# Kernel tuning notes

Hardware: AMD Instinct MI355X
Metric: run time of the kernel (lower is better)

Reference implementation:

```python
import jax, jax.numpy as jnp
import numpy as np
from math import sqrt

B, S, D, H = 2, 2048, 1024, 16
HD = D // H


def setup_inputs() -> dict:
    key = jax.random.key(0)
    ks = jax.random.split(key, 5)
    std = 0.02
    return {
        "tensor_in": jax.random.normal(ks[0], (B, S, D), dtype=jnp.float32),
        "attention_mask": jnp.zeros((1, 1, S, S), dtype=jnp.float32),
        "Wq": jax.random.normal(ks[1], (D, D), dtype=jnp.float32) * std,
        "Wk": jax.random.normal(ks[2], (D, D), dtype=jnp.float32) * std,
        "Wv": jax.random.normal(ks[3], (D, D), dtype=jnp.float32) * std,
        "Wo": jax.random.normal(ks[4], (D, D), dtype=jnp.float32) * std,
    }


def reference(tensor_in, attention_mask, Wq, Wk, Wv, Wo):
    # nn.Linear(dim, dim, bias=False): y = x @ W.T, W is [out, in]
    q = tensor_in @ Wq.T  # [B,S,D]
    k = tensor_in @ Wk.T
    v = tensor_in @ Wv.T
    # split heads -> [B,H,S,HD]
    q = q.reshape(B, S, H, HD).transpose(0, 2, 1, 3)
    k = k.reshape(B, S, H, HD).transpose(0, 2, 1, 3)
    v = v.reshape(B, S, H, HD).transpose(0, 2, 1, 3)
    # scores [B,H,S,S]; note: mask added BEFORE scaling, scale = sqrt(full dim)
    scores = jnp.einsum("bhqd,bhkd->bhqk", q, k) + attention_mask
    weights = jax.nn.softmax(scores / sqrt(D), axis=-1)  # dropout = identity (eval)
    context = jnp.einsum("bhqk,bhkd->bhqd", weights, v)
    context = context.transpose(0, 2, 1, 3).reshape(B, S, D)
    return context @ Wo.T
```

## Files before the change

kernel.cpp:

```cpp
#include <hip/hip_runtime.h>

#define B_  2
#define S_  2048
#define D_  1024
#define H_  16
#define HD_ 64
#define M_  (B_*S_)

typedef __attribute__((ext_vector_type(8))) short  short8;
typedef __attribute__((ext_vector_type(4))) float  float4v;
typedef __attribute__((ext_vector_type(4))) int    int4v;
typedef __attribute__((ext_vector_type(4))) unsigned short ushort4v;

#define PSCALE 0.0450843341f

__device__ __forceinline__ unsigned int pack2_bf16(float a, float b) {
#if __has_builtin(__builtin_amdgcn_cvt_pk_bf16_f32)
    auto p = __builtin_amdgcn_cvt_pk_bf16_f32(a, b);
    return __builtin_bit_cast(unsigned int, p);
#else
    unsigned int xa = __builtin_bit_cast(unsigned int, a);
    unsigned int xb = __builtin_bit_cast(unsigned int, b);
    xa += 0x7fffu + ((xa >> 16) & 1u);
    xb += 0x7fffu + ((xb >> 16) & 1u);
    return (xa >> 16) | (xb & 0xffff0000u);
#endif
}
__device__ __forceinline__ unsigned short f_to_bf16bits(float f) {
#if __has_builtin(__builtin_amdgcn_cvt_pk_bf16_f32)
    return (unsigned short)(pack2_bf16(f, f) & 0xffffu);
#else
    unsigned int x = __builtin_bit_cast(unsigned int, f);
    x += 0x7fffu + ((x >> 16) & 1u);
    return (unsigned short)(x >> 16);
#endif
}

__device__ __forceinline__ float fast_exp2(float x) {
#if __has_builtin(__builtin_amdgcn_exp2f)
    return __builtin_amdgcn_exp2f(x);
#else
    return exp2f(x);
#endif
}

__global__ __launch_bounds__(256) void cvt_bf16(
    const float* __restrict__ X,  const float* __restrict__ Wq,
    const float* __restrict__ Wk, const float* __restrict__ Wv,
    const float* __restrict__ Wo,
    unsigned short* __restrict__ Xb,  unsigned short* __restrict__ Wqb,
    unsigned short* __restrict__ Wkb, unsigned short* __restrict__ Wvb,
    unsigned short* __restrict__ Wob)
{
    const long t = (long)blockIdx.x * 256 + threadIdx.x;
    const long e = t * 8;
    const float* src; unsigned short* dst; long off;
    if      (e < 4194304) { src = X;  dst = Xb;  off = e; }
    else if (e < 5242880) { src = Wq; dst = Wqb; off = e - 4194304; }
    else if (e < 6291456) { src = Wk; dst = Wkb; off = e - 5242880; }
    else if (e < 7340032) { src = Wv; dst = Wvb; off = e - 6291456; }
    else                  { src = Wo; dst = Wob; off = e - 7340032; }
    float4v a = *(const float4v*)&src[off];
    float4v b = *(const float4v*)&src[off + 4];
    int4v o;
    o[0] = (int)pack2_bf16(a[0], a[1]);
    o[1] = (int)pack2_bf16(a[2], a[3]);
    o[2] = (int)pack2_bf16(b[0], b[1]);
    o[3] = (int)pack2_bf16(b[2], b[3]);
    *(int4v*)&dst[off] = o;
}

__global__ __launch_bounds__(256) void gemm_bt(
    const unsigned short* __restrict__ A,
    const unsigned short* __restrict__ B0,
    const unsigned short* __restrict__ B1,
    const unsigned short* __restrict__ B2,
    void* __restrict__ O0, void* __restrict__ O1, void* __restrict__ O2,
    int mode_base)
{
    const int K = 1024;
    const int z = blockIdx.z;
    const int mode = mode_base + z;
    const unsigned short* Aop;
    const unsigned short* Bop;
    void* Op = (z == 0) ? O0 : (z == 1) ? O1 : O2;
    int m0, n0;
    if (mode == 2) {
        Aop = B2; Bop = A;
        m0 = blockIdx.y * 128;
        n0 = blockIdx.x * 128;
    } else {
        Aop = A;
        Bop = (z == 0) ? B0 : (z == 1) ? B1 : B2;
        m0 = blockIdx.x * 128;
        n0 = blockIdx.y * 128;
    }

    __shared__ alignas(16) unsigned short As[128 * 64];
    __shared__ alignas(16) unsigned short Bs[128 * 64];

    const int tid  = threadIdx.x;
    const int wv   = tid >> 6;
    const int lane = tid & 63;
    const int wm   = wv >> 1, wn = wv & 1;
    const int q4   = lane >> 4, l15 = lane & 15;

    const unsigned short* gA[4];
    const unsigned short* gB[4];
    int ldsoff[4];
#pragma unroll
    for (int j = 0; j < 4; j++) {
        const int r = wv * 32 + j * 8 + (lane >> 3);
        const int c = (((lane & 7) ^ (r & 7)) * 8);
        gA[j] = Aop + (long)(m0 + r) * K + c;
        gB[j] = Bop + (long)(n0 + r) * K + c;
        ldsoff[j] = (wv * 32 + j * 8) * 64 + lane * 8;
    }

    int aoff[2][4], boff[2][4];
#pragma unroll
    for (int ks = 0; ks < 2; ks++)
#pragma unroll
        for (int t = 0; t < 4; t++) {
            const int swz = (((ks * 4 + q4) ^ (l15 & 7)) * 8);
            aoff[ks][t] = (wm * 64 + t * 16 + l15) * 64 + swz;
            boff[ks][t] = (wn * 64 + t * 16 + l15) * 64 + swz;
        }

    float4v acc[4][4];
#pragma unroll
    for (int i = 0; i < 4; i++)
#pragma unroll
        for (int j = 0; j < 4; j++) acc[i][j] = (float4v)0.0f;

    int4v ar[4], br[4];
#pragma unroll
    for (int j = 0; j < 4; j++) {
        ar[j] = *(const int4v*)gA[j];
        br[j] = *(const int4v*)gB[j];
        gA[j] += 64; gB[j] += 64;
    }

    for (int k0 = 0; k0 < K; k0 += 64) {
        __syncthreads();
#pragma unroll
        for (int j = 0; j < 4; j++) {
            *(int4v*)&As[ldsoff[j]] = ar[j];
            *(int4v*)&Bs[ldsoff[j]] = br[j];
        }
        __syncthreads();

        if (k0 + 64 < K) {
#pragma unroll
            for (int j = 0; j < 4; j++) {
                ar[j] = *(const int4v*)gA[j];
                br[j] = *(const int4v*)gB[j];
                gA[j] += 64; gB[j] += 64;
            }
        }

#pragma unroll
        for (int ks = 0; ks < 2; ks++) {
            short8 afr[4], bfr[4];
#pragma unroll
            for (int mt = 0; mt < 4; mt++) afr[mt] = *(const short8*)&As[aoff[ks][mt]];
#pragma unroll
            for (int nt = 0; nt < 4; nt++) bfr[nt] = *(const short8*)&Bs[boff[ks][nt]];
#pragma unroll
            for (int mt = 0; mt < 4; mt++)
#pragma unroll
                for (int nt = 0; nt < 4; nt++)
                    acc[mt][nt] = __builtin_amdgcn_mfma_f32_16x16x32_bf16(
                        afr[mt], bfr[nt], acc[mt][nt], 0, 0, 0);
        }
    }

#pragma unroll
    for (int mt = 0; mt < 4; mt++)
#pragma unroll
        for (int nt = 0; nt < 4; nt++)
#pragma unroll
            for (int r = 0; r < 4; r++) {
                const int m = m0 + wm * 64 + mt * 16 + q4 * 4 + r;
                const int n = n0 + wn * 64 + nt * 16 + l15;
                float v = acc[mt][nt][r];
                if (mode == 3) {
                    ((float*)Op)[(long)m * D_ + n] = v;
                } else if (mode == 2) {
                    const long off = (((long)(n >> 11) * H_ + (m >> 6)) * HD_ + (m & 63)) * S_ + (n & 2047);
                    ((unsigned short*)Op)[off] = f_to_bf16bits(v);
                } else {
                    const long off = ((long)((m >> 11) * H_ + (n >> 6)) * S_ + (m & 2047)) * HD_ + (n & 63);
                    if (mode == 0) v *= PSCALE;
                    ((unsigned short*)Op)[off] = f_to_bf16bits(v);
                }
            }
}

__global__ __launch_bounds__(128) void attn(
    const unsigned short* __restrict__ Q,
    const unsigned short* __restrict__ Kk,
    const unsigned short* __restrict__ Vt,
    const float* __restrict__ mask,
    unsigned short* __restrict__ ctx)
{
    __shared__ alignas(16) unsigned short Ks [64 * 72];
    __shared__ alignas(16) unsigned short Vts[64 * 72];
    __shared__ alignas(16) unsigned short Ps [2][32 * 72];

    const int tid  = threadIdx.x;
    const int wv   = tid >> 6;
    const int lane = tid & 63;
    const int q4   = lane >> 4, l15 = lane & 15;
    const int bh   = blockIdx.y;
    const int q0   = blockIdx.x * 64;

    const long head = (long)bh * S_ * HD_;

    short8 qfr[2][2];
#pragma unroll
    for (int mt = 0; mt < 2; mt++) {
        const int qrow = q0 + wv * 32 + mt * 16 + l15;
        qfr[mt][0] = *(const short8*)&Q[head + (long)qrow * HD_ + q4 * 8];
        qfr[mt][1] = *(const short8*)&Q[head + (long)qrow * HD_ + 32 + q4 * 8];
    }

    float l_acc[2][4];
#pragma unroll
    for (int mt = 0; mt < 2; mt++)
#pragma unroll
        for (int r = 0; r < 4; r++) l_acc[mt][r] = 0.0f;
    float4v oacc[2][4];
#pragma unroll
    for (int mt = 0; mt < 2; mt++)
#pragma unroll
        for (int dt = 0; dt < 4; dt++) oacc[mt][dt] = (float4v)0.0f;

    const int srow = tid >> 3;
    const int scol = (tid & 7) * 8;
    const unsigned short* gK[4];
    const unsigned short* gV[4];
    int ldsOff[4];
#pragma unroll
    for (int j = 0; j < 4; j++) {
        const int row = j * 16 + srow;
        gK[j] = Kk + head + (long)row * HD_ + scol;
        gV[j] = Vt + head + (long)row * S_  + scol;
        ldsOff[j] = row * 72 + scol;
    }

    const float* mrow[2][4];
#pragma unroll
    for (int mt = 0; mt < 2; mt++)
#pragma unroll
        for (int r = 0; r < 4; r++)
            mrow[mt][r] = mask + (long)(q0 + wv * 32 + mt * 16 + q4 * 4 + r) * S_ + l15;

    for (int k0 = 0; k0 < S_; k0 += 64) {
        __syncthreads();
#pragma unroll
        for (int j = 0; j < 4; j++) {
            *(int4v*)&Ks [ldsOff[j]] = *(const int4v*)(gK[j] + (long)k0 * HD_);
            *(int4v*)&Vts[ldsOff[j]] = *(const int4v*)(gV[j] + k0);
        }
        __syncthreads();

        float mv[2][4][4];
#pragma unroll
        for (int mt = 0; mt < 2; mt++)
#pragma unroll
            for (int nt = 0; nt < 4; nt++)
#pragma unroll
                for (int r = 0; r < 4; r++)
                    mv[mt][nt][r] = mrow[mt][r][k0 + nt * 16];

        float4v sfr[2][4];
#pragma unroll
        for (int nt = 0; nt < 4; nt++) {
            short8 kb0 = *(const short8*)&Ks[(nt * 16 + l15) * 72 + q4 * 8];
            short8 kb1 = *(const short8*)&Ks[(nt * 16 + l15) * 72 + 32 + q4 * 8];
#pragma unroll
            for (int mt = 0; mt < 2; mt++) {
                float4v s = (float4v)0.0f;
                s = __builtin_amdgcn_mfma_f32_16x16x32_bf16(qfr[mt][0], kb0, s, 0, 0, 0);
                s = __builtin_amdgcn_mfma_f32_16x16x32_bf16(qfr[mt][1], kb1, s, 0, 0, 0);
                sfr[mt][nt] = s;
            }
        }

#pragma unroll
        for (int mt = 0; mt < 2; mt++)
#pragma unroll
            for (int nt = 0; nt < 4; nt++)
#pragma unroll
                for (int r = 0; r < 4; r++) {
                    const float p = fast_exp2(fmaf(mv[mt][nt][r], PSCALE, sfr[mt][nt][r]));
                    l_acc[mt][r] += p;
                    Ps[wv][(mt * 16 + q4 * 4 + r) * 72 + nt * 16 + l15] = f_to_bf16bits(p);
                }

        short8 pf[2][2];
#pragma unroll
        for (int mt = 0; mt < 2; mt++) {
            pf[mt][0] = *(const short8*)&Ps[wv][(mt * 16 + l15) * 72 + q4 * 8];
            pf[mt][1] = *(const short8*)&Ps[wv][(mt * 16 + l15) * 72 + 32 + q4 * 8];
        }

#pragma unroll
        for (int dt = 0; dt < 4; dt++) {
            short8 vb0 = *(const short8*)&Vts[(dt * 16 + l15) * 72 + q4 * 8];
            short8 vb1 = *(const short8*)&Vts[(dt * 16 + l15) * 72 + 32 + q4 * 8];
#pragma unroll
            for (int mt = 0; mt < 2; mt++) {
                float4v o = oacc[mt][dt];
                o = __builtin_amdgcn_mfma_f32_16x16x32_bf16(pf[mt][0], vb0, o, 0, 0, 0);
                o = __builtin_amdgcn_mfma_f32_16x16x32_bf16(pf[mt][1], vb1, o, 0, 0, 0);
                oacc[mt][dt] = o;
            }
        }
    }

#pragma unroll
    for (int mt = 0; mt < 2; mt++)
#pragma unroll
        for (int r = 0; r < 4; r++) {
#pragma unroll
            for (int off = 1; off < 16; off <<= 1)
                l_acc[mt][r] += __shfl_xor(l_acc[mt][r], off);
        }

    const int b = bh >> 4, h = bh & 15;
#pragma unroll
    for (int mt = 0; mt < 2; mt++)
#pragma unroll
        for (int dt = 0; dt < 4; dt++)
#pragma unroll
            for (int r = 0; r < 4; r++) {
                const int qg = q0 + wv * 32 + mt * 16 + q4 * 4 + r;
                const int d  = dt * 16 + l15;
                const float v = oacc[mt][dt][r] / l_acc[mt][r];
                ctx[((long)(b * S_ + qg)) * D_ + h * HD_ + d] = f_to_bf16bits(v);
            }
}

extern "C" void kernel_launch(void* const* d_in, const int* in_sizes, int n_in,
                              void* d_out, int out_size, void* d_ws, size_t ws_size,
                              hipStream_t stream) {
    const float* X    = (const float*)d_in[0];
    const float* mask = (const float*)d_in[1];
    const float* Wq   = (const float*)d_in[2];
    const float* Wk   = (const float*)d_in[3];
    const float* Wv   = (const float*)d_in[4];
    const float* Wo   = (const float*)d_in[5];
    float* out        = (float*)d_out;

    unsigned short* ws = (unsigned short*)d_ws;
    unsigned short* qws  = ws;
    unsigned short* kws  = ws + 4194304;
    unsigned short* vtws = ws + 8388608;
    unsigned short* ctx  = ws + 12582912;
    unsigned short* Xb   = ws + 16777216;
    unsigned short* Wqb  = ws + 20971520;
    unsigned short* Wkb  = ws + 22020096;
    unsigned short* Wvb  = ws + 23068672;
    unsigned short* Wob  = ws + 24117248;

    cvt_bf16<<<dim3(4096), 256, 0, stream>>>(X, Wq, Wk, Wv, Wo, Xb, Wqb, Wkb, Wvb, Wob);
    gemm_bt<<<dim3(32, 8, 3), 256, 0, stream>>>(Xb, Wqb, Wkb, Wvb, qws, kws, vtws, 0);
    attn<<<dim3(32, 32, 1), 128, 0, stream>>>(qws, kws, vtws, mask, ctx);
    gemm_bt<<<dim3(32, 8, 1), 256, 0, stream>>>(ctx, Wob, Wob, Wob, out, out, out, 3);
}
```

Before: 225.6 us.

## Keep softmax probabilities in registers via permlane swaps and prefetch K/V tiles

The attention kernel now computes S transposed (K as the A operand). Each lane then holds four consecutive key columns, so probabilities are packed to bf16 in registers and rearranged with permlane32/16 swaps into the PV MFMA A-operand layout. This removes the per-wave LDS round trip for P. The next K/V tile is also prefetched into registers during compute, and mask loads become float4 vector loads. The row-sum reduction and final normalization are reworked to match the new layout, which adds register pressure and depends on the permlane builtins being available, otherwise falling back to shuffles.

Measured after the change: 231.5 us. 1.03x slower.

```diff
diff --git a/kernel.cpp b/kernel.cpp
--- a/kernel.cpp
+++ b/kernel.cpp
@@ -41,6 +41,25 @@
     return __builtin_amdgcn_exp2f(x);
 #else
     return exp2f(x);
+#endif
+}
+
+__device__ __forceinline__ void plswap(unsigned int a, unsigned int b,
+                                       unsigned int& lo, unsigned int& hi) {
+#if __has_builtin(__builtin_amdgcn_permlane32_swap) && __has_builtin(__builtin_amdgcn_permlane16_swap)
+    auto t = __builtin_amdgcn_permlane32_swap(a, b, false, false);
+    auto u = __builtin_amdgcn_permlane16_swap(t[0], t[1], false, false);
+    lo = u[0]; hi = u[1];
+#else
+    const int lane = (int)(threadIdx.x & 63);
+    unsigned int bx = __shfl_xor(b, 32);
+    unsigned int ax = __shfl_xor(a, 32);
+    unsigned int t0 = (lane & 32) ? bx : a;
+    unsigned int t1 = (lane & 32) ? b  : ax;
+    unsigned int t0x = __shfl_xor(t0, 16);
+    unsigned int t1x = __shfl_xor(t1, 16);
+    lo = (lane & 16) ? t1x : t0;
+    hi = (lane & 16) ? t1  : t0x;
 #endif
 }
 
@@ -206,7 +225,6 @@
 {
     __shared__ alignas(16) unsigned short Ks [64 * 72];
     __shared__ alignas(16) unsigned short Vts[64 * 72];
-    __shared__ alignas(16) unsigned short Ps [2][32 * 72];
 
     const int tid  = threadIdx.x;
     const int wv   = tid >> 6;
@@ -225,11 +243,7 @@
         qfr[mt][1] = *(const short8*)&Q[head + (long)qrow * HD_ + 32 + q4 * 8];
     }
 
-    float l_acc[2][4];
-#pragma unroll
-    for (int mt = 0; mt < 2; mt++)
-#pragma unroll
-        for (int r = 0; r < 4; r++) l_acc[mt][r] = 0.0f;
+    float l_acc[2] = {0.0f, 0.0f};
     float4v oacc[2][4];
 #pragma unroll
     for (int mt = 0; mt < 2; mt++)
@@ -249,30 +263,41 @@
         ldsOff[j] = row * 72 + scol;
     }
 
-    const float* mrow[2][4];
+    const float* mrowp[2];
 #pragma unroll
     for (int mt = 0; mt < 2; mt++)
-#pragma unroll
-        for (int r = 0; r < 4; r++)
-            mrow[mt][r] = mask + (long)(q0 + wv * 32 + mt * 16 + q4 * 4 + r) * S_ + l15;
+        mrowp[mt] = mask + (long)(q0 + wv * 32 + mt * 16 + l15) * S_ + q4 * 4;
+
+    int4v kreg[4], vreg[4];
+#pragma unroll
+    for (int j = 0; j < 4; j++) {
+        kreg[j] = *(const int4v*)gK[j];
+        vreg[j] = *(const int4v*)gV[j];
+    }
 
     for (int k0 = 0; k0 < S_; k0 += 64) {
         __syncthreads();
 #pragma unroll
         for (int j = 0; j < 4; j++) {
-            *(int4v*)&Ks [ldsOff[j]] = *(const int4v*)(gK[j] + (long)k0 * HD_);
-            *(int4v*)&Vts[ldsOff[j]] = *(const int4v*)(gV[j] + k0);
+            *(int4v*)&Ks [ldsOff[j]] = kreg[j];
+            *(int4v*)&Vts[ldsOff[j]] = vreg[j];
         }
         __syncthreads();
 
-        float mv[2][4][4];
+        if (k0 + 64 < S_) {
+#pragma unroll
+            for (int j = 0; j < 4; j++) {
+                kreg[j] = *(const int4v*)(gK[j] + (long)(k0 + 64) * HD_);
+                vreg[j] = *(const int4v*)(gV[j] + (k0 + 64));
+            }
+        }
+
+        float4v mv[2][4];
 #pragma unroll
         for (int mt = 0; mt < 2; mt++)
 #pragma unroll
             for (int nt = 0; nt < 4; nt++)
-#pragma unroll
-                for (int r = 0; r < 4; r++)
-                    mv[mt][nt][r] = mrow[mt][r][k0 + nt * 16];
+                mv[mt][nt] = *(const float4v*)(mrowp[mt] + k0 + nt * 16);
 
         float4v sfr[2][4];
 #pragma unroll
@@ -282,28 +307,35 @@
 #pragma unroll
             for (int mt = 0; mt < 2; mt++) {
                 float4v s = (float4v)0.0f;
-                s = __builtin_amdgcn_mfma_f32_16x16x32_bf16(qfr[mt][0], kb0, s, 0, 0, 0);
-                s = __builtin_amdgcn_mfma_f32_16x16x32_bf16(qfr[mt][1], kb1, s, 0, 0, 0);
+                s = __builtin_amdgcn_mfma_f32_16x16x32_bf16(kb0, qfr[mt][0], s, 0, 0, 0);
+                s = __builtin_amdgcn_mfma_f32_16x16x32_bf16(kb1, qfr[mt][1], s, 0, 0, 0);
                 sfr[mt][nt] = s;
             }
         }
 
-#pragma unroll
-        for (int mt = 0; mt < 2; mt++)
-#pragma unroll
-            for (int nt = 0; nt < 4; nt++)
-#pragma unroll
-                for (int r = 0; r < 4; r++) {
-                    const float p = fast_exp2(fmaf(mv[mt][nt][r], PSCALE, sfr[mt][nt][r]));
-                    l_acc[mt][r] += p;
-                    Ps[wv][(mt * 16 + q4 * 4 + r) * 72 + nt * 16 + l15] = f_to_bf16bits(p);
-                }
-
-        short8 pf[2][2];
+        short8 pa[2][2];
 #pragma unroll
         for (int mt = 0; mt < 2; mt++) {
-            pf[mt][0] = *(const short8*)&Ps[wv][(mt * 16 + l15) * 72 + q4 * 8];
-            pf[mt][1] = *(const short8*)&Ps[wv][(mt * 16 + l15) * 72 + 32 + q4 * 8];
+            unsigned int w[4][2];
+#pragma unroll
+            for (int nt = 0; nt < 4; nt++) {
+                float pv0 = fast_exp2(fmaf(mv[mt][nt][0], PSCALE, sfr[mt][nt][0]));
+                float pv1 = fast_exp2(fmaf(mv[mt][nt][1], PSCALE, sfr[mt][nt][1]));
+                float pv2 = fast_exp2(fmaf(mv[mt][nt][2], PSCALE, sfr[mt][nt][2]));
+                float pv3 = fast_exp2(fmaf(mv[mt][nt][3], PSCALE, sfr[mt][nt][3]));
+                l_acc[mt] += (pv0 + pv1) + (pv2 + pv3);
+                w[nt][0] = pack2_bf16(pv0, pv1);
+                w[nt][1] = pack2_bf16(pv2, pv3);
+            }
+#pragma unroll
+            for (int kk = 0; kk < 2; kk++) {
+                unsigned int d0, d1, d2, d3;
+                plswap(w[2 * kk][0], w[2 * kk + 1][0], d0, d2);
+                plswap(w[2 * kk][1], w[2 * kk + 1][1], d1, d3);
+                int4v pw;
+                pw[0] = (int)d0; pw[1] = (int)d1; pw[2] = (int)d2; pw[3] = (int)d3;
+                pa[mt][kk] = __builtin_bit_cast(short8, pw);
+            }
         }
 
 #pragma unroll
@@ -313,34 +345,36 @@
 #pragma unroll
             for (int mt = 0; mt < 2; mt++) {
                 float4v o = oacc[mt][dt];
-                o = __builtin_amdgcn_mfma_f32_16x16x32_bf16(pf[mt][0], vb0, o, 0, 0, 0);
-                o = __builtin_amdgcn_mfma_f32_16x16x32_bf16(pf[mt][1], vb1, o, 0, 0, 0);
+                o = __builtin_amdgcn_mfma_f32_16x16x32_bf16(pa[mt][0], vb0, o, 0, 0, 0);
+                o = __builtin_amdgcn_mfma_f32_16x16x32_bf16(pa[mt][1], vb1, o, 0, 0, 0);
                 oacc[mt][dt] = o;
             }
         }
     }
 
 #pragma unroll
-    for (int mt = 0; mt < 2; mt++)
-#pragma unroll
-        for (int r = 0; r < 4; r++) {
-#pragma unroll
-            for (int off = 1; off < 16; off <<= 1)
-                l_acc[mt][r] += __shfl_xor(l_acc[mt][r], off);
-        }
+    for (int mt = 0; mt < 2; mt++) {
+        l_acc[mt] += __shfl_xor(l_acc[mt], 16);
+        l_acc[mt] += __shfl_xor(l_acc[mt], 32);
+    }
 
     const int b = bh >> 4, h = bh & 15;
 #pragma unroll
-    for (int mt = 0; mt < 2; mt++)
+    for (int mt = 0; mt < 2; mt++) {
+        float lr[4];
+#pragma unroll
+        for (int r = 0; r < 4; r++)
+            lr[r] = __shfl(l_acc[mt], q4 * 4 + r, 16);
 #pragma unroll
         for (int dt = 0; dt < 4; dt++)
 #pragma unroll
             for (int r = 0; r < 4; r++) {
                 const int qg = q0 + wv * 32 + mt * 16 + q4 * 4 + r;
                 const int d  = dt * 16 + l15;
-                const float v = oacc[mt][dt][r] / l_acc[mt][r];
+                const float v = oacc[mt][dt][r] / lr[r];
                 ctx[((long)(b * S_ + qg)) * D_ + h * HD_ + d] = f_to_bf16bits(v);
             }
+    }
 }
 
 extern "C" void kernel_launch(void* const* d_in, const int* in_sizes, int n_in,
```

## Fuse fp32-to-bf16 conversion into GEMM loads and enlarge attention blocks

Applied to the files above, without the earlier changes.

Removes the separate conversion kernel: the GEMMs now read fp32 X and weights directly and convert to bf16 in registers while staging into shared memory. This saves a launch and a round trip of bf16 copies through global memory, but the GEMMs now read twice the bytes per tile and redo weight conversion for every tile. The attention kernel also moves from 2 to 4 waves per block (128 query rows), so each K/V tile loaded into shared memory is reused by more queries, at the cost of fewer blocks and more shared memory per block.

Result: slower. 263.5 us (+16.8%).

```diff
diff --git a/kernel.cpp b/kernel.cpp
--- a/kernel.cpp
+++ b/kernel.cpp
@@ -10,7 +10,6 @@
 typedef __attribute__((ext_vector_type(8))) short  short8;
 typedef __attribute__((ext_vector_type(4))) float  float4v;
 typedef __attribute__((ext_vector_type(4))) int    int4v;
-typedef __attribute__((ext_vector_type(4))) unsigned short ushort4v;
 
 #define PSCALE 0.0450843341f
 
@@ -44,45 +43,20 @@
 #endif
 }
 
-__global__ __launch_bounds__(256) void cvt_bf16(
-    const float* __restrict__ X,  const float* __restrict__ Wq,
-    const float* __restrict__ Wk, const float* __restrict__ Wv,
-    const float* __restrict__ Wo,
-    unsigned short* __restrict__ Xb,  unsigned short* __restrict__ Wqb,
-    unsigned short* __restrict__ Wkb, unsigned short* __restrict__ Wvb,
-    unsigned short* __restrict__ Wob)
-{
-    const long t = (long)blockIdx.x * 256 + threadIdx.x;
-    const long e = t * 8;
-    const float* src; unsigned short* dst; long off;
-    if      (e < 4194304) { src = X;  dst = Xb;  off = e; }
-    else if (e < 5242880) { src = Wq; dst = Wqb; off = e - 4194304; }
-    else if (e < 6291456) { src = Wk; dst = Wkb; off = e - 5242880; }
-    else if (e < 7340032) { src = Wv; dst = Wvb; off = e - 6291456; }
-    else                  { src = Wo; dst = Wob; off = e - 7340032; }
-    float4v a = *(const float4v*)&src[off];
-    float4v b = *(const float4v*)&src[off + 4];
-    int4v o;
-    o[0] = (int)pack2_bf16(a[0], a[1]);
-    o[1] = (int)pack2_bf16(a[2], a[3]);
-    o[2] = (int)pack2_bf16(b[0], b[1]);
-    o[3] = (int)pack2_bf16(b[2], b[3]);
-    *(int4v*)&dst[off] = o;
-}
-
+template<bool AF32, bool BF32>
 __global__ __launch_bounds__(256) void gemm_bt(
-    const unsigned short* __restrict__ A,
-    const unsigned short* __restrict__ B0,
-    const unsigned short* __restrict__ B1,
-    const unsigned short* __restrict__ B2,
+    const void* __restrict__ A,
+    const void* __restrict__ B0,
+    const void* __restrict__ B1,
+    const void* __restrict__ B2,
     void* __restrict__ O0, void* __restrict__ O1, void* __restrict__ O2,
     int mode_base)
 {
     const int K = 1024;
     const int z = blockIdx.z;
     const int mode = mode_base + z;
-    const unsigned short* Aop;
-    const unsigned short* Bop;
+    const void* Aop;
+    const void* Bop;
     void* Op = (z == 0) ? O0 : (z == 1) ? O1 : O2;
     int m0, n0;
     if (mode == 2) {
@@ -105,17 +79,47 @@
     const int wm   = wv >> 1, wn = wv & 1;
     const int q4   = lane >> 4, l15 = lane & 15;
 
-    const unsigned short* gA[4];
-    const unsigned short* gB[4];
+    long offA[4], offB[4];
     int ldsoff[4];
 #pragma unroll
     for (int j = 0; j < 4; j++) {
         const int r = wv * 32 + j * 8 + (lane >> 3);
         const int c = (((lane & 7) ^ (r & 7)) * 8);
-        gA[j] = Aop + (long)(m0 + r) * K + c;
-        gB[j] = Bop + (long)(n0 + r) * K + c;
+        offA[j] = (long)(m0 + r) * K + c;
+        offB[j] = (long)(n0 + r) * K + c;
         ldsoff[j] = (wv * 32 + j * 8) * 64 + lane * 8;
     }
+
+    auto ldA = [&](int j, long k) -> int4v {
+        if constexpr (AF32) {
+            const float* p = (const float*)Aop + offA[j] + k;
+            float4v a = *(const float4v*)p;
+            float4v b = *(const float4v*)(p + 4);
+            int4v o;
+            o[0] = (int)pack2_bf16(a[0], a[1]);
+            o[1] = (int)pack2_bf16(a[2], a[3]);
+            o[2] = (int)pack2_bf16(b[0], b[1]);
+            o[3] = (int)pack2_bf16(b[2], b[3]);
+            return o;
+        } else {
+            return *(const int4v*)((const unsigned short*)Aop + offA[j] + k);
+        }
+    };
+    auto ldB = [&](int j, long k) -> int4v {
+        if constexpr (BF32) {
+            const float* p = (const float*)Bop + offB[j] + k;
+            float4v a = *(const float4v*)p;
+            float4v b = *(const float4v*)(p + 4);
+            int4v o;
+            o[0] = (int)pack2_bf16(a[0], a[1]);
+            o[1] = (int)pack2_bf16(a[2], a[3]);
+            o[2] = (int)pack2_bf16(b[0], b[1]);
+            o[3] = (int)pack2_bf16(b[2], b[3]);
+            return o;
+        } else {
+            return *(const int4v*)((const unsigned short*)Bop + offB[j] + k);
+        }
+    };
 
     int aoff[2][4], boff[2][4];
 #pragma unroll
@@ -136,9 +140,8 @@
     int4v ar[4], br[4];
 #pragma unroll
     for (int j = 0; j < 4; j++) {
-        ar[j] = *(const int4v*)gA[j];
-        br[j] = *(const int4v*)gB[j];
-        gA[j] += 64; gB[j] += 64;
+        ar[j] = ldA(j, 0);
+        br[j] = ldB(j, 0);
     }
 
     for (int k0 = 0; k0 < K; k0 += 64) {
@@ -153,9 +156,8 @@
         if (k0 + 64 < K) {
 #pragma unroll
             for (int j = 0; j < 4; j++) {
-                ar[j] = *(const int4v*)gA[j];
-                br[j] = *(const int4v*)gB[j];
-                gA[j] += 64; gB[j] += 64;
+                ar[j] = ldA(j, k0 + 64);
+                br[j] = ldB(j, k0 + 64);
             }
         }
 
@@ -197,7 +199,7 @@
             }
 }
 
-__global__ __launch_bounds__(128) void attn(
+__global__ __launch_bounds__(256) void attn(
     const unsigned short* __restrict__ Q,
     const unsigned short* __restrict__ Kk,
     const unsigned short* __restrict__ Vt,
@@ -206,14 +208,14 @@
 {
     __shared__ alignas(16) unsigned short Ks [64 * 72];
     __shared__ alignas(16) unsigned short Vts[64 * 72];
-    __shared__ alignas(16) unsigned short Ps [2][32 * 72];
+    __shared__ alignas(16) unsigned short Ps [4][32 * 72];
 
     const int tid  = threadIdx.x;
     const int wv   = tid >> 6;
     const int lane = tid & 63;
     const int q4   = lane >> 4, l15 = lane & 15;
     const int bh   = blockIdx.y;
-    const int q0   = blockIdx.x * 64;
+    const int q0   = blockIdx.x * 128;
 
     const long head = (long)bh * S_ * HD_;
 
@@ -238,12 +240,12 @@
 
     const int srow = tid >> 3;
     const int scol = (tid & 7) * 8;
-    const unsigned short* gK[4];
-    const unsigned short* gV[4];
-    int ldsOff[4];
-#pragma unroll
-    for (int j = 0; j < 4; j++) {
-        const int row = j * 16 + srow;
+    const unsigned short* gK[2];
+    const unsigned short* gV[2];
+    int ldsOff[2];
+#pragma unroll
+    for (int j = 0; j < 2; j++) {
+        const int row = j * 32 + srow;
         gK[j] = Kk + head + (long)row * HD_ + scol;
         gV[j] = Vt + head + (long)row * S_  + scol;
         ldsOff[j] = row * 72 + scol;
@@ -259,7 +261,7 @@
     for (int k0 = 0; k0 < S_; k0 += 64) {
         __syncthreads();
 #pragma unroll
-        for (int j = 0; j < 4; j++) {
+        for (int j = 0; j < 2; j++) {
             *(int4v*)&Ks [ldsOff[j]] = *(const int4v*)(gK[j] + (long)k0 * HD_);
             *(int4v*)&Vts[ldsOff[j]] = *(const int4v*)(gV[j] + k0);
         }
@@ -359,14 +361,10 @@
     unsigned short* kws  = ws + 4194304;
     unsigned short* vtws = ws + 8388608;
     unsigned short* ctx  = ws + 12582912;
-    unsigned short* Xb   = ws + 16777216;
-    unsigned short* Wqb  = ws + 20971520;
-    unsigned short* Wkb  = ws + 22020096;
-    unsigned short* Wvb  = ws + 23068672;
-    unsigned short* Wob  = ws + 24117248;
-
-    cvt_bf16<<<dim3(4096), 256, 0, stream>>>(X, Wq, Wk, Wv, Wo, Xb, Wqb, Wkb, Wvb, Wob);
-    gemm_bt<<<dim3(32, 8, 3), 256, 0, stream>>>(Xb, Wqb, Wkb, Wvb, qws, kws, vtws, 0);
-    attn<<<dim3(32, 32, 1), 128, 0, stream>>>(qws, kws, vtws, mask, ctx);
-    gemm_bt<<<dim3(32, 8, 1), 256, 0, stream>>>(ctx, Wob, Wob, Wob, out, out, out, 3);
-}
+
+    gemm_bt<true, true><<<dim3(32, 8, 3), 256, 0, stream>>>(
+        X, Wq, Wk, Wv, qws, kws, vtws, 0);
+    attn<<<dim3(16, 32, 1), 256, 0, stream>>>(qws, kws, vtws, mask, ctx);
+    gemm_bt<false, true><<<dim3(32, 8, 1), 256, 0, stream>>>(
+        ctx, Wo, Wo, Wo, out, out, out, 3);
+}
```

## Double-buffer K/V tiles with register prefetch and use 4-wave attention blocks

Applied to the files above, without the earlier changes.

The attention kernel now uses 256-thread blocks covering 128 query rows, so each K/V tile loaded into shared memory serves twice as many queries. K/V tiles are prefetched into registers for the next iteration and written into alternating shared buffers, cutting one barrier per iteration and overlapping global loads with MFMA work. Shared memory per block grows and the grid halves, which may reduce occupancy or the number of blocks per CU.

Measured after the change: 224.7 us. About the same (-0.4%).

```diff
diff --git a/kernel.cpp b/kernel.cpp
--- a/kernel.cpp
+++ b/kernel.cpp
@@ -10,7 +10,6 @@
 typedef __attribute__((ext_vector_type(8))) short  short8;
 typedef __attribute__((ext_vector_type(4))) float  float4v;
 typedef __attribute__((ext_vector_type(4))) int    int4v;
-typedef __attribute__((ext_vector_type(4))) unsigned short ushort4v;
 
 #define PSCALE 0.0450843341f
 
@@ -197,23 +196,23 @@
             }
 }
 
-__global__ __launch_bounds__(128) void attn(
+__global__ __launch_bounds__(256) void attn(
     const unsigned short* __restrict__ Q,
     const unsigned short* __restrict__ Kk,
     const unsigned short* __restrict__ Vt,
     const float* __restrict__ mask,
     unsigned short* __restrict__ ctx)
 {
-    __shared__ alignas(16) unsigned short Ks [64 * 72];
-    __shared__ alignas(16) unsigned short Vts[64 * 72];
-    __shared__ alignas(16) unsigned short Ps [2][32 * 72];
+    __shared__ alignas(16) unsigned short Ks [2][64 * 72];
+    __shared__ alignas(16) unsigned short Vts[2][64 * 72];
+    __shared__ alignas(16) unsigned short Ps [4][32 * 72];
 
     const int tid  = threadIdx.x;
     const int wv   = tid >> 6;
     const int lane = tid & 63;
     const int q4   = lane >> 4, l15 = lane & 15;
     const int bh   = blockIdx.y;
-    const int q0   = blockIdx.x * 64;
+    const int q0   = blockIdx.x * 128;
 
     const long head = (long)bh * S_ * HD_;
 
@@ -238,12 +237,12 @@
 
     const int srow = tid >> 3;
     const int scol = (tid & 7) * 8;
-    const unsigned short* gK[4];
-    const unsigned short* gV[4];
-    int ldsOff[4];
-#pragma unroll
-    for (int j = 0; j < 4; j++) {
-        const int row = j * 16 + srow;
+    const unsigned short* gK[2];
+    const unsigned short* gV[2];
+    int ldsOff[2];
+#pragma unroll
+    for (int j = 0; j < 2; j++) {
+        const int row = j * 32 + srow;
         gK[j] = Kk + head + (long)row * HD_ + scol;
         gV[j] = Vt + head + (long)row * S_  + scol;
         ldsOff[j] = row * 72 + scol;
@@ -256,14 +255,31 @@
         for (int r = 0; r < 4; r++)
             mrow[mt][r] = mask + (long)(q0 + wv * 32 + mt * 16 + q4 * 4 + r) * S_ + l15;
 
-    for (int k0 = 0; k0 < S_; k0 += 64) {
+    int4v kreg[2], vreg[2];
+#pragma unroll
+    for (int j = 0; j < 2; j++) {
+        kreg[j] = *(const int4v*)gK[j];
+        vreg[j] = *(const int4v*)gV[j];
+    }
+
+    for (int it = 0; it < S_ / 64; it++) {
+        const int k0  = it * 64;
+        const int buf = it & 1;
+
+#pragma unroll
+        for (int j = 0; j < 2; j++) {
+            *(int4v*)&Ks [buf][ldsOff[j]] = kreg[j];
+            *(int4v*)&Vts[buf][ldsOff[j]] = vreg[j];
+        }
         __syncthreads();
-#pragma unroll
-        for (int j = 0; j < 4; j++) {
-            *(int4v*)&Ks [ldsOff[j]] = *(const int4v*)(gK[j] + (long)k0 * HD_);
-            *(int4v*)&Vts[ldsOff[j]] = *(const int4v*)(gV[j] + k0);
-        }
-        __syncthreads();
+
+        if (it + 1 < S_ / 64) {
+#pragma unroll
+            for (int j = 0; j < 2; j++) {
+                kreg[j] = *(const int4v*)(gK[j] + (long)(k0 + 64) * HD_);
+                vreg[j] = *(const int4v*)(gV[j] + (k0 + 64));
+            }
+        }
 
         float mv[2][4][4];
 #pragma unroll
@@ -277,8 +293,8 @@
         float4v sfr[2][4];
 #pragma unroll
         for (int nt = 0; nt < 4; nt++) {
-            short8 kb0 = *(const short8*)&Ks[(nt * 16 + l15) * 72 + q4 * 8];
-            short8 kb1 = *(const short8*)&Ks[(nt * 16 + l15) * 72 + 32 + q4 * 8];
+            short8 kb0 = *(const short8*)&Ks[buf][(nt * 16 + l15) * 72 + q4 * 8];
+            short8 kb1 = *(const short8*)&Ks[buf][(nt * 16 + l15) * 72 + 32 + q4 * 8];
 #pragma unroll
             for (int mt = 0; mt < 2; mt++) {
                 float4v s = (float4v)0.0f;
@@ -308,8 +324,8 @@
 
 #pragma unroll
         for (int dt = 0; dt < 4; dt++) {
-            short8 vb0 = *(const short8*)&Vts[(dt * 16 + l15) * 72 + q4 * 8];
-            short8 vb1 = *(const short8*)&Vts[(dt * 16 + l15) * 72 + 32 + q4 * 8];
+            short8 vb0 = *(const short8*)&Vts[buf][(dt * 16 + l15) * 72 + q4 * 8];
+            short8 vb1 = *(const short8*)&Vts[buf][(dt * 16 + l15) * 72 + 32 + q4 * 8];
 #pragma unroll
             for (int mt = 0; mt < 2; mt++) {
                 float4v o = oacc[mt][dt];
@@ -367,6 +383,6 @@
 
     cvt_bf16<<<dim3(4096), 256, 0, stream>>>(X, Wq, Wk, Wv, Wo, Xb, Wqb, Wkb, Wvb, Wob);
     gemm_bt<<<dim3(32, 8, 3), 256, 0, stream>>>(Xb, Wqb, Wkb, Wvb, qws, kws, vtws, 0);
-    attn<<<dim3(32, 32, 1), 128, 0, stream>>>(qws, kws, vtws, mask, ctx);
+    attn<<<dim3(16, 32, 1), 256, 0, stream>>>(qws, kws, vtws, mask, ctx);
     gemm_bt<<<dim3(32, 8, 1), 256, 0, stream>>>(ctx, Wob, Wob, Wob, out, out, out, 3);
 }
```
